# Kernel optimization log

Measured on AMD Instinct MI355X. Metric: run time of the kernel, lower is better.

The kernel has to match this reference:

```python
import jax, jax.numpy as jnp
import numpy as np

NUM_HEADS = 16
HEAD_DIM = 64  # hidden 1024 / 16


def setup_inputs() -> dict:
    key = jax.random.key(0)
    k1, k2, k3 = jax.random.split(key, 3)
    B, S, H = 2, 2048, 1024
    return {
        "hidden_states": jax.random.normal(k1, (B, S, H), dtype=jnp.float32),
        "attention_mask": jnp.zeros((B, 1, 1, S), dtype=jnp.float32),
        "c_attn_w": jax.random.normal(k2, (H, 3 * H), dtype=jnp.float32) * 0.02,
        "c_attn_b": jnp.zeros((3 * H,), dtype=jnp.float32),
        "c_proj_w": jax.random.normal(k3, (H, H), dtype=jnp.float32) * 0.02,
        "c_proj_b": jnp.zeros((H,), dtype=jnp.float32),
    }


def reference(hidden_states, attention_mask, c_attn_w, c_attn_b, c_proj_w, c_proj_b):
    B, S, H = hidden_states.shape
    nH, hd = NUM_HEADS, HEAD_DIM
    # Conv1D: x @ w + b (HF weight layout is (in, out))
    qkv = hidden_states @ c_attn_w + c_attn_b  # [B,S,3H]
    q, k, v = jnp.split(qkv, 3, axis=-1)
    # split heads -> [B,nH,S,hd]
    def heads(t):
        return t.reshape(B, S, nH, hd).transpose(0, 2, 1, 3)
    q, k, v = heads(q), heads(k), heads(v)
    scores = jnp.einsum("bhqd,bhkd->bhqk", q, k) / np.sqrt(hd).astype(jnp.float32)
    scores = scores + attention_mask  # additive mask, broadcast [B,1,1,S]
    attn = jax.nn.softmax(scores, axis=-1)  # dropout is identity (eval)
    ctx = jnp.einsum("bhqk,bhkd->bhqd", attn, v)
    ctx = ctx.transpose(0, 2, 1, 3).reshape(B, S, H)  # merge heads
    out = ctx @ c_proj_w + c_proj_b
    return out
```

## Files before the change

kernel.cpp:

```cpp
#include <hip/hip_runtime.h>
#include <hip/hip_bf16.h>

typedef __attribute__((ext_vector_type(8))) short short8;
typedef __attribute__((ext_vector_type(4))) float f32x4;

__device__ __forceinline__ unsigned short f2bf(float f) {
  union { __hip_bfloat16 h; unsigned short u; } cv;
  cv.h = __float2bfloat16(f);
  return cv.u;
}

__device__ __forceinline__ void gld16(const void* g, void* l) {
  __builtin_amdgcn_global_load_lds(
      (const __attribute__((address_space(1))) unsigned int*)g,
      (__attribute__((address_space(3))) unsigned int*)l, 16, 0, 0);
}

__device__ __forceinline__ f32x4 mfma_bf16(short8 a, short8 b, f32x4 c) {
  return __builtin_amdgcn_mfma_f32_16x16x32_bf16(a, b, c, 0, 0, 0);
}

#define QSCALE 0.18033688011112042f
#define L2E    1.4426950408889634f

__global__ void prep(const float* __restrict__ x, unsigned short* __restrict__ xbf,
                     const float* __restrict__ wa, unsigned short* __restrict__ da,
                     const float* __restrict__ wp, unsigned short* __restrict__ dp) {
  __shared__ float tile[64][65];
  const int t = threadIdx.x;
  const int bid = blockIdx.x;
  if (bid < 4096) {
    int i = bid * 256 + t;
    float4 v = ((const float4*)x)[i];
    ushort4 o;
    o.x = f2bf(v.x); o.y = f2bf(v.y); o.z = f2bf(v.z); o.w = f2bf(v.w);
    ((ushort4*)xbf)[i] = o;
    return;
  }
  int idx = bid - 4096;
  const int tr = idx & 15;
  int y = idx >> 4;
  const float* src;
  unsigned short* dst;
  int C;
  if (y < 48) { src = wa; dst = da; C = 3072; }
  else        { src = wp; dst = dp; C = 1024; y -= 48; }
  const int tc = y;
#pragma unroll
  for (int i = 0; i < 16; ++i) {
    int id2 = t + i * 256;
    int lr = id2 >> 6, lc = id2 & 63;
    tile[lr][lc] = src[(size_t)(tr * 64 + lr) * C + tc * 64 + lc];
  }
  __syncthreads();
#pragma unroll
  for (int i = 0; i < 16; ++i) {
    int id2 = t + i * 256;
    int lr = id2 >> 6, lc = id2 & 63;
    dst[(size_t)(tc * 64 + lr) * 1024 + tr * 64 + lc] = f2bf(tile[lc][lr]);
  }
}

template <int KDIM>
__device__ __forceinline__ void gemm_core(const short* __restrict__ A, const short* __restrict__ Bt,
                                          int mbase, int nbase, short* As, short* Bs,
                                          int wm, int wn, int quad, int l16, int t,
                                          f32x4 (&acc)[4][4]) {
  for (int kt = 0; kt < KDIM / 32; ++kt) {
#pragma unroll
    for (int i = 0; i < 2; ++i) {
      int c = t + i * 256;
      int row = c >> 2, c4 = c & 3;
      gld16(A + (size_t)(mbase + row) * KDIM + kt * 32 + c4 * 8, (char*)As + c * 16);
      gld16(Bt + (size_t)(nbase + row) * KDIM + kt * 32 + c4 * 8, (char*)Bs + c * 16);
    }
    __syncthreads();
    short8 af[4], bf[4];
#pragma unroll
    for (int m = 0; m < 4; ++m)
      af[m] = *(const short8*)((const char*)As + (wm + m * 16 + l16) * 64 + quad * 16);
#pragma unroll
    for (int n = 0; n < 4; ++n)
      bf[n] = *(const short8*)((const char*)Bs + (wn + n * 16 + l16) * 64 + quad * 16);
#pragma unroll
    for (int m = 0; m < 4; ++m)
#pragma unroll
      for (int n = 0; n < 4; ++n)
        acc[m][n] = mfma_bf16(af[m], bf[n], acc[m][n]);
    __syncthreads();
  }
}

__global__ __launch_bounds__(256, 2) void gemm_qkv(
    const short* __restrict__ A, const short* __restrict__ Bt, const float* __restrict__ bias,
    unsigned short* __restrict__ q, unsigned short* __restrict__ k,
    unsigned short* __restrict__ vt) {
  __shared__ __align__(16) char smem[17408];
  short* As = (short*)smem;
  short* Bs = (short*)(smem + 8192);
  unsigned short* vlds = (unsigned short*)smem;
  const int t = threadIdx.x;
  const int wave = t >> 6, lane = t & 63;
  const int quad = lane >> 4, l16 = lane & 15;
  const int wm = (wave >> 1) * 64, wn = (wave & 1) * 64;
  const int mbase = blockIdx.x * 128, nbase = blockIdx.y * 128;
  f32x4 acc[4][4];
#pragma unroll
  for (int i = 0; i < 4; ++i)
#pragma unroll
    for (int j = 0; j < 4; ++j) acc[i][j] = (f32x4)0.0f;
  gemm_core<1024>(A, Bt, mbase, nbase, As, Bs, wm, wn, quad, l16, t, acc);

  if (nbase < 2048) {
#pragma unroll
    for (int n = 0; n < 4; ++n) {
      int col = nbase + wn + n * 16 + l16;
      float bc = bias[col];
      int which = col >> 10, rem = col & 1023;
      int h = rem >> 6, d = rem & 63;
      unsigned short* dst = which ? k : q;
      float scale = which ? 1.0f : QSCALE;
#pragma unroll
      for (int m = 0; m < 4; ++m) {
#pragma unroll
        for (int r = 0; r < 4; ++r) {
          int row = mbase + wm + m * 16 + quad * 4 + r;
          int b = row >> 11, s = row & 2047;
          dst[(((size_t)(b * 16 + h)) * 2048 + s) * 64 + d] = f2bf((acc[m][n][r] + bc) * scale);
        }
      }
    }
  } else {
    const int b = mbase >> 11, s0 = mbase & 2047;
    const int vcb = nbase - 2048;
    __syncthreads();
#pragma unroll
    for (int half = 0; half < 2; ++half) {
      if (wn == half * 64) {
#pragma unroll
        for (int n = 0; n < 4; ++n) {
          int col_l = n * 16 + l16;
          float bc = bias[nbase + half * 64 + col_l];
#pragma unroll
          for (int m = 0; m < 4; ++m)
#pragma unroll
            for (int r = 0; r < 4; ++r) {
              int row_l = wm + m * 16 + quad * 4 + r;
              int idx = (row_l & 64) + ((row_l >> 5) & 1) * 32 +
                        ((row_l >> 2) & 3) * 8 + ((row_l >> 4) & 1) * 4 + (row_l & 3);
              vlds[col_l * 136 + idx] = f2bf(acc[m][n][r] + bc);
            }
        }
      }
      __syncthreads();
      int h = (vcb + half * 64) >> 6;
      size_t obase = ((size_t)(b * 16 + h)) * 64 * 2048;
#pragma unroll
      for (int i = 0; i < 4; ++i) {
        int c = t + i * 256;
        int d_l = c >> 4, c16 = c & 15;
        short8 v = *(const short8*)&vlds[d_l * 136 + c16 * 8];
        *(short8*)&vt[obase + (size_t)d_l * 2048 + s0 + c16 * 8] = v;
      }
      __syncthreads();
    }
  }
}

__global__ __launch_bounds__(256, 2) void gemm_proj(
    const short* __restrict__ A, const short* __restrict__ Bt, const float* __restrict__ bias,
    float* __restrict__ out) {
  __shared__ __align__(16) short As[64 * 32];
  __shared__ __align__(16) short Bs[128 * 32];
  const int t = threadIdx.x;
  const int wave = t >> 6, lane = t & 63;
  const int quad = lane >> 4, l16 = lane & 15;
  const int wm = (wave >> 1) * 32, wn = (wave & 1) * 64;
  const int mbase = blockIdx.x * 64, nbase = blockIdx.y * 128;
  f32x4 acc[2][4];
#pragma unroll
  for (int i = 0; i < 2; ++i)
#pragma unroll
    for (int j = 0; j < 4; ++j) acc[i][j] = (f32x4)0.0f;
  for (int kt = 0; kt < 32; ++kt) {
    {
      int row = t >> 2, c4 = t & 3;
      gld16(A + (size_t)(mbase + row) * 1024 + kt * 32 + c4 * 8, (char*)As + t * 16);
    }
#pragma unroll
    for (int i = 0; i < 2; ++i) {
      int c = t + i * 256;
      int row = c >> 2, c4 = c & 3;
      gld16(Bt + (size_t)(nbase + row) * 1024 + kt * 32 + c4 * 8, (char*)Bs + c * 16);
    }
    __syncthreads();
    short8 af[2], bf[4];
#pragma unroll
    for (int m = 0; m < 2; ++m)
      af[m] = *(const short8*)((const char*)As + (wm + m * 16 + l16) * 64 + quad * 16);
#pragma unroll
    for (int n = 0; n < 4; ++n)
      bf[n] = *(const short8*)((const char*)Bs + (wn + n * 16 + l16) * 64 + quad * 16);
#pragma unroll
    for (int m = 0; m < 2; ++m)
#pragma unroll
      for (int n = 0; n < 4; ++n)
        acc[m][n] = mfma_bf16(af[m], bf[n], acc[m][n]);
    __syncthreads();
  }
#pragma unroll
  for (int n = 0; n < 4; ++n) {
    int col = nbase + wn + n * 16 + l16;
    float bc = bias[col];
#pragma unroll
    for (int m = 0; m < 2; ++m)
#pragma unroll
      for (int r = 0; r < 4; ++r) {
        int row = mbase + wm + m * 16 + quad * 4 + r;
        out[(size_t)row * 1024 + col] = acc[m][n][r] + bc;
      }
  }
}

__global__ __launch_bounds__(256, 2) void flash_attn(
    const short* __restrict__ Qg, const short* __restrict__ Kg, const short* __restrict__ Vtg,
    const float* __restrict__ mask, unsigned short* __restrict__ ctx) {
  __shared__ __align__(16) unsigned char smem[49152];
  const int t = threadIdx.x;
  const int wave = t >> 6, lane = t & 63;
  const int quad = lane >> 4, l16 = lane & 15;
  const int bh = blockIdx.x, b = bh >> 4, h = bh & 15;
  const int qbase = blockIdx.y * 128;
  const size_t bh_off = (size_t)bh * 2048 * 64;

#pragma unroll
  for (int i = 0; i < 4; ++i) {
    int c = t + i * 256;
    int row = c >> 3, col = c & 7;
    gld16(Qg + bh_off + (size_t)(qbase + row) * 64 + (col ^ (row & 7)) * 8,
          (char*)smem + c * 16);
  }
  __syncthreads();
  short8 qf[2][2];
#pragma unroll
  for (int mf = 0; mf < 2; ++mf)
#pragma unroll
    for (int ks = 0; ks < 2; ++ks) {
      int row = wave * 32 + mf * 16 + l16;
      qf[mf][ks] = *(const short8*)((const char*)smem +
                                    (row * 8 + ((ks * 4 + quad) ^ (l16 & 7))) * 16);
    }
  __syncthreads();

  int koff[2][4];
#pragma unroll
  for (int ks = 0; ks < 2; ++ks)
#pragma unroll
    for (int n = 0; n < 4; ++n) {
      int row = n * 16 + l16;
      koff[ks][n] = (row * 8 + ((ks * 4 + quad) ^ (l16 & 7))) * 16;
    }
  int voff[2][4];
#pragma unroll
  for (int ks = 0; ks < 2; ++ks)
#pragma unroll
    for (int db = 0; db < 4; ++db) {
      int d = db * 16 + l16;
      voff[ks][db] = d * 128 + (((ks * 4 + quad) ^ (d & 7)) * 16);
    }

  const short* kgp[2];
  const short* vgp[2];
#pragma unroll
  for (int i = 0; i < 2; ++i) {
    int c = t + i * 256;
    int row = c >> 3, col = c & 7;
    kgp[i] = Kg + bh_off + (size_t)row * 64 + (col ^ (row & 7)) * 8;
    vgp[i] = Vtg + ((size_t)bh * 64 + row) * 2048 + (col ^ (row & 7)) * 8;
  }
  const float* mpt = mask + b * 2048 + quad * 4;

  auto stage_to = [&](char* kd, char* vd) {
#pragma unroll
    for (int i = 0; i < 2; ++i) {
      gld16(kgp[i], kd + (t + i * 256) * 16);
      gld16(vgp[i], vd + (t + i * 256) * 16);
    }
    kgp[0] += 4096; kgp[1] += 4096;
    vgp[0] += 64;   vgp[1] += 64;
  };

  f32x4 O[2][4];
  float l_part[2];
#pragma unroll
  for (int mf = 0; mf < 2; ++mf)
#pragma unroll
    for (int d = 0; d < 4; ++d) O[mf][d] = (f32x4)0.0f;
  l_part[0] = 0.0f;
  l_part[1] = 0.0f;

  char* const KB[3] = {(char*)smem, (char*)smem + 8192, (char*)smem + 16384};
  char* const VB[3] = {(char*)smem + 24576, (char*)smem + 32768, (char*)smem + 40960};

  auto iter_body = [&](const char* Kc, const char* Vc, char* ksd, char* vsd,
                       bool doStage) {
    __builtin_amdgcn_s_barrier();
    __builtin_amdgcn_sched_barrier(0);

    float4 mq[4];
#pragma unroll
    for (int n = 0; n < 4; ++n) mq[n] = *(const float4*)(mpt + n * 16);
    mpt += 64;
    __builtin_amdgcn_sched_barrier(0);

    if (doStage) stage_to(ksd, vsd);

    f32x4 sa[2][4];
    __builtin_amdgcn_s_setprio(1);
#pragma unroll
    for (int n = 0; n < 4; ++n) {
      short8 kf = *(const short8*)(Kc + koff[0][n]);
      sa[0][n] = mfma_bf16(kf, qf[0][0], (f32x4)0.0f);
      sa[1][n] = mfma_bf16(kf, qf[1][0], (f32x4)0.0f);
    }
#pragma unroll
    for (int n = 0; n < 4; ++n) {
      short8 kf = *(const short8*)(Kc + koff[1][n]);
      sa[0][n] = mfma_bf16(kf, qf[0][1], sa[0][n]);
      sa[1][n] = mfma_bf16(kf, qf[1][1], sa[1][n]);
    }
    __builtin_amdgcn_s_setprio(0);

    short8 pa[2][2];
#pragma unroll
    for (int mf = 0; mf < 2; ++mf) {
      float rs = 0.0f;
#pragma unroll
      for (int n = 0; n < 4; ++n) {
#pragma unroll
        for (int r = 0; r < 4; ++r) {
          float p = __builtin_amdgcn_exp2f(__builtin_fmaf(mq[n][r], L2E, sa[mf][n][r]));
          rs += p;
          pa[mf][n >> 1][(n & 1) * 4 + r] = (short)f2bf(p);
        }
      }
      l_part[mf] += rs;
    }

    __builtin_amdgcn_s_setprio(1);
#pragma unroll
    for (int ks = 0; ks < 2; ++ks) {
#pragma unroll
      for (int db = 0; db < 4; ++db) {
        short8 vf = *(const short8*)(Vc + voff[ks][db]);
        O[0][db] = mfma_bf16(pa[0][ks], vf, O[0][db]);
        O[1][db] = mfma_bf16(pa[1][ks], vf, O[1][db]);
      }
    }
    __builtin_amdgcn_s_setprio(0);
  };

  stage_to(KB[0], VB[0]);
  stage_to(KB[1], VB[1]);

#define VMW4 asm volatile("s_waitcnt vmcnt(4)" ::: "memory")
#define VMW0 asm volatile("s_waitcnt vmcnt(0)" ::: "memory")

#pragma unroll 1
  for (int kt3 = 0; kt3 < 30; kt3 += 3) {
    VMW4; iter_body(KB[0], VB[0], KB[2], VB[2], true);
    VMW4; iter_body(KB[1], VB[1], KB[0], VB[0], true);
    VMW4; iter_body(KB[2], VB[2], KB[1], VB[1], true);
  }
  VMW4; iter_body(KB[0], VB[0], nullptr, nullptr, false);
  VMW0; iter_body(KB[1], VB[1], nullptr, nullptr, false);

#undef VMW4
#undef VMW0

  float lr[2];
#pragma unroll
  for (int mf = 0; mf < 2; ++mf) {
    float l = l_part[mf];
    l += __shfl_xor(l, 16);
    l += __shfl_xor(l, 32);
    lr[mf] = l;
  }
#pragma unroll
  for (int mf = 0; mf < 2; ++mf) {
#pragma unroll
    for (int r = 0; r < 4; ++r) {
      float lq = __shfl(lr[mf], quad * 4 + r);
      float inv = 1.0f / lq;
      int s = qbase + wave * 32 + mf * 16 + quad * 4 + r;
      size_t o = ((size_t)b * 2048 + s) * 1024 + h * 64;
#pragma unroll
      for (int db = 0; db < 4; ++db)
        ctx[o + db * 16 + l16] = f2bf(O[mf][db][r] * inv);
    }
  }
}

extern "C" void kernel_launch(void* const* d_in, const int* in_sizes, int n_in,
                              void* d_out, int out_size, void* d_ws, size_t ws_size,
                              hipStream_t stream) {
  const float* x      = (const float*)d_in[0];
  const float* mask   = (const float*)d_in[1];
  const float* w_attn = (const float*)d_in[2];
  const float* b_attn = (const float*)d_in[3];
  const float* w_proj = (const float*)d_in[4];
  const float* b_proj = (const float*)d_in[5];
  float* out = (float*)d_out;

  char* ws = (char*)d_ws;
  const size_t MB = 1024 * 1024;
  short*          Xbf    = (short*)(ws);
  short*          Wqkv_t = (short*)(ws + 8 * MB);
  short*          Wprj_t = (short*)(ws + 14 * MB);
  unsigned short* Qb     = (unsigned short*)(ws + 16 * MB);
  unsigned short* Kb     = (unsigned short*)(ws + 24 * MB);
  unsigned short* Vtb    = (unsigned short*)(ws + 32 * MB);
  unsigned short* ctx    = (unsigned short*)Xbf;

  prep<<<5120, 256, 0, stream>>>(x, (unsigned short*)Xbf,
                                 w_attn, (unsigned short*)Wqkv_t,
                                 w_proj, (unsigned short*)Wprj_t);
  gemm_qkv<<<dim3(32, 24), 256, 0, stream>>>(Xbf, Wqkv_t, b_attn, Qb, Kb, Vtb);
  flash_attn<<<dim3(32, 16), 256, 0, stream>>>((const short*)Qb, (const short*)Kb,
                                               (const short*)Vtb, mask, ctx);
  gemm_proj<<<dim3(64, 8), 256, 0, stream>>>((const short*)ctx, Wprj_t, b_proj, out);
}
```

Measured before the change: 178.8 us.

## Double-buffer LDS in QKV and proj GEMMs and vectorize permuted bf16 stores

The QKV and projection GEMMs now use two LDS buffers, so the next K-tile's global_load_lds is issued while MFMAs run on the current tile, with one barrier per tile instead of two. The Q/K epilogue and the flash-attention context store now pack four bf16 values into one 8-byte store. To make this valid, the head dimension (and ctx columns) is stored in a permuted order, and the proj weight conversion permutes its input rows to match. This relies on the permutation staying consistent across kernels and raises LDS use in the QKV kernel to 32 KB.

```diff
diff --git a/kernel.cpp b/kernel.cpp
--- a/kernel.cpp
+++ b/kernel.cpp
@@ -2,6 +2,7 @@
 #include <hip/hip_bf16.h>
 
 typedef __attribute__((ext_vector_type(8))) short short8;
+typedef __attribute__((ext_vector_type(4))) short short4v;
 typedef __attribute__((ext_vector_type(4))) float f32x4;
 
 __device__ __forceinline__ unsigned short f2bf(float f) {
@@ -45,6 +46,7 @@
   int C;
   if (y < 48) { src = wa; dst = da; C = 3072; }
   else        { src = wp; dst = dp; C = 1024; y -= 48; }
+  const int pflag = (C == 1024);
   const int tc = y;
 #pragma unroll
   for (int i = 0; i < 16; ++i) {
@@ -57,37 +59,8 @@
   for (int i = 0; i < 16; ++i) {
     int id2 = t + i * 256;
     int lr = id2 >> 6, lc = id2 & 63;
-    dst[(size_t)(tc * 64 + lr) * 1024 + tr * 64 + lc] = f2bf(tile[lc][lr]);
-  }
-}
-
-template <int KDIM>
-__device__ __forceinline__ void gemm_core(const short* __restrict__ A, const short* __restrict__ Bt,
-                                          int mbase, int nbase, short* As, short* Bs,
-                                          int wm, int wn, int quad, int l16, int t,
-                                          f32x4 (&acc)[4][4]) {
-  for (int kt = 0; kt < KDIM / 32; ++kt) {
-#pragma unroll
-    for (int i = 0; i < 2; ++i) {
-      int c = t + i * 256;
-      int row = c >> 2, c4 = c & 3;
-      gld16(A + (size_t)(mbase + row) * KDIM + kt * 32 + c4 * 8, (char*)As + c * 16);
-      gld16(Bt + (size_t)(nbase + row) * KDIM + kt * 32 + c4 * 8, (char*)Bs + c * 16);
-    }
-    __syncthreads();
-    short8 af[4], bf[4];
-#pragma unroll
-    for (int m = 0; m < 4; ++m)
-      af[m] = *(const short8*)((const char*)As + (wm + m * 16 + l16) * 64 + quad * 16);
-#pragma unroll
-    for (int n = 0; n < 4; ++n)
-      bf[n] = *(const short8*)((const char*)Bs + (wn + n * 16 + l16) * 64 + quad * 16);
-#pragma unroll
-    for (int m = 0; m < 4; ++m)
-#pragma unroll
-      for (int n = 0; n < 4; ++n)
-        acc[m][n] = mfma_bf16(af[m], bf[n], acc[m][n]);
-    __syncthreads();
+    int lcs = pflag ? ((lc & 15) * 4 + (lc >> 4)) : lc;
+    dst[(size_t)(tc * 64 + lr) * 1024 + tr * 64 + lcs] = f2bf(tile[lc][lr]);
   }
 }
 
@@ -95,9 +68,11 @@
     const short* __restrict__ A, const short* __restrict__ Bt, const float* __restrict__ bias,
     unsigned short* __restrict__ q, unsigned short* __restrict__ k,
     unsigned short* __restrict__ vt) {
-  __shared__ __align__(16) char smem[17408];
-  short* As = (short*)smem;
-  short* Bs = (short*)(smem + 8192);
+  __shared__ __align__(16) char smem[32768];
+  char* const A0 = smem;
+  char* const A1 = smem + 8192;
+  char* const B0 = smem + 16384;
+  char* const B1 = smem + 24576;
   unsigned short* vlds = (unsigned short*)smem;
   const int t = threadIdx.x;
   const int wave = t >> 6, lane = t & 63;
@@ -109,25 +84,72 @@
   for (int i = 0; i < 4; ++i)
 #pragma unroll
     for (int j = 0; j < 4; ++j) acc[i][j] = (f32x4)0.0f;
-  gemm_core<1024>(A, Bt, mbase, nbase, As, Bs, wm, wn, quad, l16, t, acc);
+
+  const short* ap[2];
+  const short* bp[2];
+#pragma unroll
+  for (int i = 0; i < 2; ++i) {
+    int c = t + i * 256;
+    int row = c >> 2, c4 = c & 3;
+    ap[i] = A + (size_t)(mbase + row) * 1024 + c4 * 8;
+    bp[i] = Bt + (size_t)(nbase + row) * 1024 + c4 * 8;
+  }
+  auto stg = [&](char* as, char* bs) {
+#pragma unroll
+    for (int i = 0; i < 2; ++i) {
+      int c = t + i * 256;
+      gld16(ap[i], as + c * 16);
+      gld16(bp[i], bs + c * 16);
+    }
+    ap[0] += 32; ap[1] += 32; bp[0] += 32; bp[1] += 32;
+  };
+  auto cmp = [&](const char* as, const char* bs) {
+    short8 af[4], bf[4];
+#pragma unroll
+    for (int m = 0; m < 4; ++m)
+      af[m] = *(const short8*)(as + (wm + m * 16 + l16) * 64 + quad * 16);
+#pragma unroll
+    for (int n = 0; n < 4; ++n)
+      bf[n] = *(const short8*)(bs + (wn + n * 16 + l16) * 64 + quad * 16);
+#pragma unroll
+    for (int m = 0; m < 4; ++m)
+#pragma unroll
+      for (int n = 0; n < 4; ++n)
+        acc[m][n] = mfma_bf16(af[m], bf[n], acc[m][n]);
+  };
+
+  stg(A0, B0);
+  __syncthreads();
+#pragma unroll 1
+  for (int kt = 0; kt < 32; kt += 2) {
+    stg(A1, B1);
+    cmp(A0, B0);
+    __syncthreads();
+    if (kt + 2 < 32) stg(A0, B0);
+    cmp(A1, B1);
+    __syncthreads();
+  }
 
   if (nbase < 2048) {
-#pragma unroll
-    for (int n = 0; n < 4; ++n) {
-      int col = nbase + wn + n * 16 + l16;
-      float bc = bias[col];
-      int which = col >> 10, rem = col & 1023;
-      int h = rem >> 6, d = rem & 63;
-      unsigned short* dst = which ? k : q;
-      float scale = which ? 1.0f : QSCALE;
-#pragma unroll
-      for (int m = 0; m < 4; ++m) {
-#pragma unroll
-        for (int r = 0; r < 4; ++r) {
-          int row = mbase + wm + m * 16 + quad * 4 + r;
-          int b = row >> 11, s = row & 2047;
-          dst[(((size_t)(b * 16 + h)) * 2048 + s) * 64 + d] = f2bf((acc[m][n][r] + bc) * scale);
-        }
+    const int colbase = nbase + wn;
+    const int which = colbase >> 10;
+    const int h = (colbase & 1023) >> 6;
+    unsigned short* dst = which ? k : q;
+    const float scale = which ? 1.0f : QSCALE;
+    float bc[4];
+#pragma unroll
+    for (int n = 0; n < 4; ++n) bc[n] = bias[colbase + n * 16 + l16];
+#pragma unroll
+    for (int m = 0; m < 4; ++m) {
+#pragma unroll
+      for (int r = 0; r < 4; ++r) {
+        int row = mbase + wm + m * 16 + quad * 4 + r;
+        int b = row >> 11, s = row & 2047;
+        short4v o;
+#pragma unroll
+        for (int n = 0; n < 4; ++n)
+          o[n] = (short)f2bf((acc[m][n][r] + bc[n]) * scale);
+        *(short4v*)&dst[(((size_t)(b * 16 + h)) * 2048 + s) * 64 + l16 * 4] = o;
       }
     }
   } else {
@@ -170,8 +192,11 @@
 __global__ __launch_bounds__(256, 2) void gemm_proj(
     const short* __restrict__ A, const short* __restrict__ Bt, const float* __restrict__ bias,
     float* __restrict__ out) {
-  __shared__ __align__(16) short As[64 * 32];
-  __shared__ __align__(16) short Bs[128 * 32];
+  __shared__ __align__(16) char smem[24576];
+  char* const A0 = smem;
+  char* const A1 = smem + 4096;
+  char* const B0 = smem + 8192;
+  char* const B1 = smem + 16384;
   const int t = threadIdx.x;
   const int wave = t >> 6, lane = t & 63;
   const int quad = lane >> 4, l16 = lane & 15;
@@ -182,32 +207,52 @@
   for (int i = 0; i < 2; ++i)
 #pragma unroll
     for (int j = 0; j < 4; ++j) acc[i][j] = (f32x4)0.0f;
-  for (int kt = 0; kt < 32; ++kt) {
-    {
-      int row = t >> 2, c4 = t & 3;
-      gld16(A + (size_t)(mbase + row) * 1024 + kt * 32 + c4 * 8, (char*)As + t * 16);
-    }
-#pragma unroll
-    for (int i = 0; i < 2; ++i) {
-      int c = t + i * 256;
-      int row = c >> 2, c4 = c & 3;
-      gld16(Bt + (size_t)(nbase + row) * 1024 + kt * 32 + c4 * 8, (char*)Bs + c * 16);
-    }
-    __syncthreads();
+
+  const short* ap;
+  const short* bp[2];
+  {
+    int row = t >> 2, c4 = t & 3;
+    ap = A + (size_t)(mbase + row) * 1024 + c4 * 8;
+  }
+#pragma unroll
+  for (int i = 0; i < 2; ++i) {
+    int c = t + i * 256;
+    int row = c >> 2, c4 = c & 3;
+    bp[i] = Bt + (size_t)(nbase + row) * 1024 + c4 * 8;
+  }
+  auto stg = [&](char* as, char* bs) {
+    gld16(ap, as + t * 16);
+#pragma unroll
+    for (int i = 0; i < 2; ++i) gld16(bp[i], bs + (t + i * 256) * 16);
+    ap += 32; bp[0] += 32; bp[1] += 32;
+  };
+  auto cmp = [&](const char* as, const char* bs) {
     short8 af[2], bf[4];
 #pragma unroll
     for (int m = 0; m < 2; ++m)
-      af[m] = *(const short8*)((const char*)As + (wm + m * 16 + l16) * 64 + quad * 16);
+      af[m] = *(const short8*)(as + (wm + m * 16 + l16) * 64 + quad * 16);
 #pragma unroll
     for (int n = 0; n < 4; ++n)
-      bf[n] = *(const short8*)((const char*)Bs + (wn + n * 16 + l16) * 64 + quad * 16);
+      bf[n] = *(const short8*)(bs + (wn + n * 16 + l16) * 64 + quad * 16);
 #pragma unroll
     for (int m = 0; m < 2; ++m)
 #pragma unroll
       for (int n = 0; n < 4; ++n)
         acc[m][n] = mfma_bf16(af[m], bf[n], acc[m][n]);
+  };
+
+  stg(A0, B0);
+  __syncthreads();
+#pragma unroll 1
+  for (int kt = 0; kt < 32; kt += 2) {
+    stg(A1, B1);
+    cmp(A0, B0);
     __syncthreads();
-  }
+    if (kt + 2 < 32) stg(A0, B0);
+    cmp(A1, B1);
+    __syncthreads();
+  }
+
 #pragma unroll
   for (int n = 0; n < 4; ++n) {
     int col = nbase + wn + n * 16 + l16;
@@ -394,9 +439,11 @@
       float inv = 1.0f / lq;
       int s = qbase + wave * 32 + mf * 16 + quad * 4 + r;
       size_t o = ((size_t)b * 2048 + s) * 1024 + h * 64;
+      short4v o4;
 #pragma unroll
       for (int db = 0; db < 4; ++db)
-        ctx[o + db * 16 + l16] = f2bf(O[mf][db][r] * inv);
+        o4[db] = (short)f2bf(O[mf][db][r] * inv);
+      *(short4v*)&ctx[o + l16 * 4] = o4;
     }
   }
 }
```

Measured after the change: 181.0 us. No clear change (+1.2%).
